# Optimization experiments

Measured on AMD Instinct MI355X. Metric: run time of the kernel, lower is better.

Reference implementation:

```python
import jax, jax.numpy as jnp
import numpy as np

B, MAXN, NVT, NINP, NHID, NHEAD, NL, NZ = 1024, 32, 16, 256, 512, 8, 6, 64
HID = MAXN * NHID
EPS = 1e-5
SCALE = 1.0 / np.sqrt(NHID // NHEAD)


def setup_inputs() -> dict:
    key = jax.random.key(0)
    ks = jax.random.split(key, 16)
    s = 0.02
    d = {}
    d["node_types"] = jax.random.randint(ks[0], (B, MAXN), 0, NVT, dtype=jnp.int32)
    d["adj_bits"] = jax.random.randint(ks[1], (B, MAXN, MAXN), 0, 2, dtype=jnp.int32)
    d["Wpos"] = jax.random.normal(ks[2], (MAXN, NINP), jnp.float32) * s
    d["bpos"] = jnp.zeros((NINP,), jnp.float32)
    d["Wnode"] = jax.random.normal(ks[3], (NVT, NINP), jnp.float32) * s
    d["bnode"] = jnp.zeros((NINP,), jnp.float32)
    for i, n in enumerate(["Wq", "Wk", "Wv", "Wo", "W1", "W2"]):
        d["enc_" + n] = jax.random.normal(ks[4 + i], (NL, NHID, NHID), jnp.float32) * s
    for n in ["bq", "bk", "bv", "bo", "b1", "b2"]:
        d["enc_" + n] = jnp.zeros((NL, NHID), jnp.float32)
    d["ln1_g"] = jnp.ones((NL, NHID), jnp.float32)
    d["ln1_b"] = jnp.zeros((NL, NHID), jnp.float32)
    d["ln2_g"] = jnp.ones((NL, NHID), jnp.float32)
    d["ln2_b"] = jnp.zeros((NL, NHID), jnp.float32)
    d["Wfc1"] = jax.random.normal(ks[10], (HID, NZ), jnp.float32) * s
    d["bfc1"] = jnp.zeros((NZ,), jnp.float32)
    d["Wfc2"] = jax.random.normal(ks[11], (HID, NZ), jnp.float32) * s
    d["bfc2"] = jnp.zeros((NZ,), jnp.float32)
    return d


def _ln(x, g, b):
    m = x.mean(-1, keepdims=True)
    v = ((x - m) ** 2).mean(-1, keepdims=True)
    return (x - m) * jax.lax.rsqrt(v + EPS) * g + b


def _dag_attn_bias(adj_bits):
    # _mask_generate: transitive closure via matmul powers; log-depth squaring
    # over a boolean semiring (min(.,1) after each add) gives identical reachability.
    iu = jnp.triu(jnp.ones((MAXN, MAXN), jnp.float32), 1)  # enforce DAG
    adj = adj_bits.astype(jnp.float32) * iu  # [B,N,N]
    reach = adj
    for _ in range(int(np.ceil(np.log2(MAXN)))):
        reach = jnp.minimum(reach + jnp.matmul(reach, reach), 1.0)
    # original: mask = (sum_powers + I) < 0.5 (True=disallowed), then transpose(1,2)
    allowed = (jnp.swapaxes(reach, 1, 2) + jnp.eye(MAXN, dtype=jnp.float32)) > 0.5
    return jnp.where(allowed, 0.0, -jnp.inf)[:, None, :, :]  # [B,1,N,N]


def _encode(node_types, adj_bits, Wpos, bpos, Wnode, bnode,
            enc_Wq, enc_bq, enc_Wk, enc_bk, enc_Wv, enc_bv, enc_Wo, enc_bo,
            ln1_g, ln1_b, enc_W1, enc_b1, enc_W2, enc_b2, ln2_g, ln2_b,
            Wfc1, bfc1, Wfc2, bfc2):
    node_feat = jax.nn.relu(Wnode[node_types] + bnode)               # [B,N,ninp]
    pos_feat = jnp.broadcast_to(Wpos + bpos, (B, MAXN, NINP))        # position = node index
    x = jnp.concatenate([node_feat, pos_feat], -1)                   # [B,N,512]
    bias = _dag_attn_bias(adj_bits)
    dh = NHID // NHEAD
    for l in range(NL):
        q = (x @ enc_Wq[l] + enc_bq[l]).reshape(B, MAXN, NHEAD, dh)
        k = (x @ enc_Wk[l] + enc_bk[l]).reshape(B, MAXN, NHEAD, dh)
        v = (x @ enc_Wv[l] + enc_bv[l]).reshape(B, MAXN, NHEAD, dh)
        s = jnp.einsum('bqhd,bkhd->bhqk', q, k) * SCALE + bias
        a = jax.nn.softmax(s, axis=-1)
        o = jnp.einsum('bhqk,bkhd->bqhd', a, v).reshape(B, MAXN, NHID)
        x = _ln(x + o @ enc_Wo[l] + enc_bo[l], ln1_g[l], ln1_b[l])    # post-LN
        f = jax.nn.relu(x @ enc_W1[l] + enc_b1[l]) @ enc_W2[l] + enc_b2[l]
        x = _ln(x + f, ln2_g[l], ln2_b[l])
    mem = x.reshape(B, HID)
    return mem @ Wfc1 + bfc1, mem @ Wfc2 + bfc2


def reference(node_types, adj_bits, Wpos, bpos, Wnode, bnode,
              enc_Wq, enc_bq, enc_Wk, enc_bk, enc_Wv, enc_bv, enc_Wo, enc_bo,
              ln1_g, ln1_b, enc_W1, enc_b1, enc_W2, enc_b2, ln2_g, ln2_b,
              Wfc1, bfc1, Wfc2, bfc2):
    return _encode(node_types, adj_bits, Wpos, bpos, Wnode, bnode,
                   enc_Wq, enc_bq, enc_Wk, enc_bk, enc_Wv, enc_bv, enc_Wo, enc_bo,
                   ln1_g, ln1_b, enc_W1, enc_b1, enc_W2, enc_b2, ln2_g, ln2_b,
                   Wfc1, bfc1, Wfc2, bfc2)
```

## Files before the change

kernel.cpp:

```cpp
#include <hip/hip_runtime.h>


typedef unsigned short u16;
typedef unsigned int u32;
typedef __attribute__((ext_vector_type(8))) short bf16x8;
typedef __attribute__((ext_vector_type(4))) float f32x4;

#define NB 1024
#define MAXN 32
#define NHID 512
#define NHEAD 8
#define NLAY 6
#define MTOT (NB * MAXN)
#define ATT_SCALE 0.125f
#define LN_EPS 1e-5f

__device__ __forceinline__ float bf2f(u16 h) { return __uint_as_float(((u32)h) << 16); }
__device__ __forceinline__ u16 f2bf(float f) {
  u32 u = __float_as_uint(f);
  return (u16)((u + 0x7fffu + ((u >> 16) & 1u)) >> 16);
}

__device__ __forceinline__ void gload16(const void* g, void* l) {
  __builtin_amdgcn_global_load_lds((const __attribute__((address_space(1))) void*)g,
                                   (__attribute__((address_space(3))) void*)l, 16, 0, 0);
}

__device__ __forceinline__ void xcd_remap(int l, int NX, int& mt, int& nt) {
  int xcd = l & 7;
  int s = l >> 3;
  int mg = s / NX;
  nt = s - mg * NX;
  mt = mg * 8 + xcd;
}

__global__ __launch_bounds__(256) void mask_k(const int* __restrict__ adj, u32* __restrict__ mask) {
  __shared__ u32 r[8][32];
  int tid = threadIdx.x;
  int g = tid >> 5, i = tid & 31;
  int b = blockIdx.x * 8 + g;
  const int* ab = adj + ((long)b * 32 + i) * 32;
  u32 m = 0;
  for (int j = i + 1; j < 32; ++j)
    if (ab[j]) m |= (1u << j);
  r[g][i] = m;
  __syncthreads();
  for (int it = 0; it < 5; ++it) {
    u32 cur = r[g][i];
    u32 acc = cur;
    #pragma unroll
    for (int j = 0; j < 32; ++j)
      if ((cur >> j) & 1u) acc |= r[g][j];
    __syncthreads();
    r[g][i] = acc;
    __syncthreads();
  }
  u32 am = 1u << i;
  #pragma unroll
  for (int k = 0; k < 32; ++k) am |= ((r[g][k] >> i) & 1u) << k;
  mask[b * 32 + i] = am;
}

__global__ __launch_bounds__(256) void embed_k(const int* __restrict__ types,
    const float* __restrict__ Wpos, const float* __restrict__ bpos,
    const float* __restrict__ Wnode, const float* __restrict__ bnode,
    u16* __restrict__ xb) {
  int i = blockIdx.x * 256 + threadIdx.x;
  int row = i >> 7, c = (i & 127) * 4;
  int b = row >> 5, n = row & 31;
  float v[4];
  if (c < 256) {
    int tp = types[b * 32 + n];
    const float* w = &Wnode[tp * 256 + c];
    #pragma unroll
    for (int j = 0; j < 4; ++j) v[j] = fmaxf(w[j] + bnode[c + j], 0.f);
  } else {
    int cc = c - 256;
    const float* w = &Wpos[n * 256 + cc];
    #pragma unroll
    for (int j = 0; j < 4; ++j) v[j] = w[j] + bpos[cc + j];
  }
  ushort4 h; h.x = f2bf(v[0]); h.y = f2bf(v[1]); h.z = f2bf(v[2]); h.w = f2bf(v[3]);
  *(ushort4*)&xb[(long)row * NHID + c] = h;
}

__global__ __launch_bounds__(256) void tconv_k(const float* __restrict__ W,
    u16* __restrict__ Wt, int n_off, int n_total) {
  __shared__ float tile[32][33];
  int l = blockIdx.z;
  int k0 = blockIdx.x * 32, n0 = blockIdx.y * 32;
  int tx = threadIdx.x & 31, ty = threadIdx.x >> 5;
  const float* src = W + (size_t)l * NHID * NHID;
  #pragma unroll
  for (int i = 0; i < 4; ++i)
    tile[ty + 8 * i][tx] = src[(size_t)(k0 + ty + 8 * i) * NHID + n0 + tx];
  __syncthreads();
  u16* dst = Wt + (size_t)l * n_total * NHID;
  #pragma unroll
  for (int i = 0; i < 4; ++i)
    dst[(size_t)(n_off + n0 + ty + 8 * i) * NHID + k0 + tx] = f2bf(tile[tx][ty + 8 * i]);
}

template <int EPI>
__global__ __launch_bounds__(256, 2) void gemm_bt(
    const u16* __restrict__ A, const u16* __restrict__ Bt,
    const float* __restrict__ bias0, const u16* __restrict__ res,
    u16* __restrict__ Cout, int N, int K) {
  __shared__ u16 As[128 * 32];
  __shared__ u16 Bs[128 * 32];
  const int tid = threadIdx.x;
  const int wave = tid >> 6, lane = tid & 63;
  int mt, nt;
  xcd_remap(blockIdx.x + gridDim.x * blockIdx.y, gridDim.x, mt, nt);
  const long m0 = (long)mt * 128;
  const int n0 = nt * 128;
  const int wr = wave >> 1, wc = wave & 1;
  const int srow = lane >> 2;
  const int sg = (lane & 3) ^ ((srow >> 1) & 3);
  const int fr = lane & 15;
  const int kq = lane >> 4;
  f32x4 acc[4][4] = {};

  const int kqx = (kq ^ ((fr >> 1) & 3)) * 8;
  for (int k0 = 0; k0 < K; k0 += 32) {
    #pragma unroll
    for (int i = 0; i < 2; ++i) {
      int c = 2 * wave + i;
      gload16(A + (m0 + 16 * c + srow) * (long)K + k0 + sg * 8, &As[c * 512]);
      gload16(Bt + (long)(n0 + 16 * c + srow) * K + k0 + sg * 8, &Bs[c * 512]);
    }
    __syncthreads();
    bf16x8 af[4], bfv[4];
    #pragma unroll
    for (int mi = 0; mi < 4; ++mi)
      af[mi] = *(const bf16x8*)&As[(wr * 64 + mi * 16 + fr) * 32 + kqx];
    #pragma unroll
    for (int ni = 0; ni < 4; ++ni)
      bfv[ni] = *(const bf16x8*)&Bs[(wc * 64 + ni * 16 + fr) * 32 + kqx];
    #pragma unroll
    for (int mi = 0; mi < 4; ++mi)
      #pragma unroll
      for (int ni = 0; ni < 4; ++ni)
        acc[mi][ni] = __builtin_amdgcn_mfma_f32_16x16x32_bf16(af[mi], bfv[ni], acc[mi][ni], 0, 0, 0);
    __syncthreads();
  }

  #pragma unroll
  for (int ni = 0; ni < 4; ++ni) {
    int n = n0 + wc * 64 + ni * 16 + fr;
    float bias = bias0[n];
    #pragma unroll
    for (int mi = 0; mi < 4; ++mi) {
      long r = m0 + wr * 64 + mi * 16 + kq * 4;
      #pragma unroll
      for (int j = 0; j < 4; ++j) {
        float v = acc[mi][ni][j] + bias;
        if (EPI == 2) v = fmaxf(v, 0.f);
        if (EPI == 3) v += bf2f(res[(r + j) * (long)N + n]);
        Cout[(r + j) * (long)N + n] = f2bf(v);
      }
    }
  }
}

template <int SWZ>
__global__ __launch_bounds__(256, 2) void gemm_qkv(
    const u16* __restrict__ A, const u16* __restrict__ Bt,
    const float* __restrict__ bq, const float* __restrict__ bk,
    const float* __restrict__ bv, u16* __restrict__ qk, u16* __restrict__ v) {
  __shared__ u16 As[128 * 32];
  __shared__ u16 Bs[128 * 32];
  const int tid = threadIdx.x;
  const int wave = tid >> 6, lane = tid & 63;
  int mt, nt;
  xcd_remap(blockIdx.x + gridDim.x * blockIdx.y, gridDim.x, mt, nt);
  const long m0 = (long)mt * 128;
  const int n0 = nt * 128;
  const int wr = wave >> 1, wc = wave & 1;
  const int srow = lane >> 2;
  const int sg = SWZ ? ((lane & 3) ^ ((srow >> 1) & 3)) : (lane & 3);
  const int fr = lane & 15;
  const int kq = lane >> 4;
  f32x4 acc[4][4] = {};

  const int kqx = SWZ ? ((kq ^ ((fr >> 1) & 3)) * 8) : (kq * 8);
  for (int k0 = 0; k0 < 512; k0 += 32) {
    #pragma unroll
    for (int i = 0; i < 2; ++i) {
      int c = 2 * wave + i;
      gload16(A + (m0 + 16 * c + srow) * 512L + k0 + sg * 8, &As[c * 512]);
      gload16(Bt + (long)(n0 + 16 * c + srow) * 512 + k0 + sg * 8, &Bs[c * 512]);
    }
    __syncthreads();
    bf16x8 af[4], bfv[4];
    #pragma unroll
    for (int mi = 0; mi < 4; ++mi)
      af[mi] = *(const bf16x8*)&As[(wr * 64 + mi * 16 + fr) * 32 + kqx];
    #pragma unroll
    for (int ni = 0; ni < 4; ++ni)
      bfv[ni] = *(const bf16x8*)&Bs[(wc * 64 + ni * 16 + fr) * 32 + kqx];
    #pragma unroll
    for (int mi = 0; mi < 4; ++mi)
      #pragma unroll
      for (int ni = 0; ni < 4; ++ni)
        acc[mi][ni] = __builtin_amdgcn_mfma_f32_16x16x32_bf16(af[mi], bfv[ni], acc[mi][ni], 0, 0, 0);
    __syncthreads();
  }

  #pragma unroll
  for (int ni = 0; ni < 4; ++ni) {
    int n = n0 + wc * 64 + ni * 16 + fr;
    float bias = (n < 512) ? bq[n] : ((n < 1024) ? bk[n - 512] : bv[n - 1024]);
    #pragma unroll
    for (int mi = 0; mi < 4; ++mi) {
      long r = m0 + wr * 64 + mi * 16 + kq * 4;
      #pragma unroll
      for (int j = 0; j < 4; ++j) {
        u16 hv = f2bf(acc[mi][ni][j] + bias);
        long rr = r + j;
        if (n < 1024) qk[rr * 1024 + n] = hv;
        else          v[rr * 512 + (n - 1024)] = hv;
      }
    }
  }
}

__global__ __launch_bounds__(256) void attn_k(const u16* __restrict__ qk,
    const u16* __restrict__ vfull, const u32* __restrict__ mask, u16* __restrict__ o) {
  __shared__ u16 vs_[4][64][40];
  __shared__ u16 p_lds[4][32][40];
  int tid = threadIdx.x;
  int w = tid >> 6, lane = tid & 63;
  int idx = blockIdx.x * 4 + w;
  int b = idx >> 3, h = idx & 7;
  const u16* qbase = qk + (long)b * 32 * 1024 + h * 64;
  const u16* kbase = qbase + 512;
  int g = lane >> 4, r = lane & 15;

  int node = lane >> 1, dh = lane & 1;
  const u16* vsrc = vfull + ((long)b * 32 + node) * 512 + h * 64 + dh * 32;
  bf16x8 vr[4];
  #pragma unroll
  for (int i = 0; i < 4; ++i) vr[i] = *(const bf16x8*)(vsrc + i * 8);

  f32x4 s[2][2] = {};
  #pragma unroll
  for (int ks = 0; ks < 2; ++ks) {
    bf16x8 kf[2], qf[2];
    #pragma unroll
    for (int mi = 0; mi < 2; ++mi)
      kf[mi] = *(const bf16x8*)(kbase + (long)(mi * 16 + r) * 1024 + ks * 32 + g * 8);
    #pragma unroll
    for (int nj = 0; nj < 2; ++nj)
      qf[nj] = *(const bf16x8*)(qbase + (long)(nj * 16 + r) * 1024 + ks * 32 + g * 8);
    #pragma unroll
    for (int mi = 0; mi < 2; ++mi)
      #pragma unroll
      for (int nj = 0; nj < 2; ++nj)
        s[mi][nj] = __builtin_amdgcn_mfma_f32_16x16x32_bf16(kf[mi], qf[nj], s[mi][nj], 0, 0, 0);
  }

  #pragma unroll
  for (int i = 0; i < 4; ++i)
    #pragma unroll
    for (int t = 0; t < 8; ++t)
      vs_[w][dh * 32 + i * 8 + t][node] = (u16)vr[i][t];

  #pragma unroll
  for (int nj = 0; nj < 2; ++nj) {
    int q = nj * 16 + r;
    u32 mk = mask[b * 32 + q];
    float vv[8];
    float mx = -1e30f;
    #pragma unroll
    for (int mi = 0; mi < 2; ++mi)
      #pragma unroll
      for (int j = 0; j < 4; ++j) {
        int k = mi * 16 + g * 4 + j;
        float val = ((mk >> k) & 1u) ? s[mi][nj][j] * ATT_SCALE : -1e30f;
        vv[mi * 4 + j] = val;
        mx = fmaxf(mx, val);
      }
    mx = fmaxf(mx, __shfl_xor(mx, 16));
    mx = fmaxf(mx, __shfl_xor(mx, 32));
    float sum = 0.f;
    #pragma unroll
    for (int i = 0; i < 8; ++i) { vv[i] = __expf(vv[i] - mx); sum += vv[i]; }
    sum += __shfl_xor(sum, 16);
    sum += __shfl_xor(sum, 32);
    float inv = 1.f / sum;
    #pragma unroll
    for (int mi = 0; mi < 2; ++mi) {
      ushort4 pk;
      pk.x = f2bf(vv[mi * 4 + 0] * inv);
      pk.y = f2bf(vv[mi * 4 + 1] * inv);
      pk.z = f2bf(vv[mi * 4 + 2] * inv);
      pk.w = f2bf(vv[mi * 4 + 3] * inv);
      *(ushort4*)&p_lds[w][q][mi * 16 + g * 4] = pk;
    }
  }

  bf16x8 pa[2];
  #pragma unroll
  for (int mi = 0; mi < 2; ++mi)
    pa[mi] = *(const bf16x8*)&p_lds[w][mi * 16 + r][g * 8];
  f32x4 oacc[2][4] = {};
  #pragma unroll
  for (int nd = 0; nd < 4; ++nd) {
    bf16x8 vf = *(const bf16x8*)&vs_[w][nd * 16 + r][g * 8];
    #pragma unroll
    for (int mi = 0; mi < 2; ++mi)
      oacc[mi][nd] = __builtin_amdgcn_mfma_f32_16x16x32_bf16(pa[mi], vf, oacc[mi][nd], 0, 0, 0);
  }
  #pragma unroll
  for (int mi = 0; mi < 2; ++mi)
    #pragma unroll
    for (int j = 0; j < 4; ++j) {
      int q = mi * 16 + g * 4 + j;
      u16* og = o + ((long)b * 32 + q) * NHID + h * 64;
      #pragma unroll
      for (int nd = 0; nd < 4; ++nd)
        og[nd * 16 + r] = f2bf(oacc[mi][nd][j]);
    }
}

__global__ __launch_bounds__(256) void ln_k(const u16* __restrict__ y,
    const float* __restrict__ g, const float* __restrict__ b, u16* __restrict__ xb) {
  int tid = threadIdx.x;
  int w = tid >> 6, lane = tid & 63;
  long row = (long)blockIdx.x * 4 + w;
  int c = lane * 8;
  long o = row * NHID + c;
  ushort4 a0 = *(const ushort4*)&y[o];
  ushort4 a1 = *(const ushort4*)&y[o + 4];
  float v[8] = {bf2f(a0.x), bf2f(a0.y), bf2f(a0.z), bf2f(a0.w),
                bf2f(a1.x), bf2f(a1.y), bf2f(a1.z), bf2f(a1.w)};
  float s = 0.f, sq = 0.f;
  #pragma unroll
  for (int j = 0; j < 8; ++j) { s += v[j]; sq += v[j] * v[j]; }
  #pragma unroll
  for (int off = 1; off < 64; off <<= 1) {
    s += __shfl_xor(s, off);
    sq += __shfl_xor(sq, off);
  }
  float mean = s * (1.f / 512.f);
  float inv = rsqrtf(sq * (1.f / 512.f) - mean * mean + LN_EPS);
  float4 ga = *(const float4*)&g[c], gb = *(const float4*)&g[c + 4];
  float4 ba = *(const float4*)&b[c], bb = *(const float4*)&b[c + 4];
  float gg[8] = {ga.x, ga.y, ga.z, ga.w, gb.x, gb.y, gb.z, gb.w};
  float bv[8] = {ba.x, ba.y, ba.z, ba.w, bb.x, bb.y, bb.z, bb.w};
  ushort4 o0, o1;
  o0.x = f2bf((v[0] - mean) * inv * gg[0] + bv[0]);
  o0.y = f2bf((v[1] - mean) * inv * gg[1] + bv[1]);
  o0.z = f2bf((v[2] - mean) * inv * gg[2] + bv[2]);
  o0.w = f2bf((v[3] - mean) * inv * gg[3] + bv[3]);
  o1.x = f2bf((v[4] - mean) * inv * gg[4] + bv[4]);
  o1.y = f2bf((v[5] - mean) * inv * gg[5] + bv[5]);
  o1.z = f2bf((v[6] - mean) * inv * gg[6] + bv[6]);
  o1.w = f2bf((v[7] - mean) * inv * gg[7] + bv[7]);
  *(ushort4*)&xb[o] = o0;
  *(ushort4*)&xb[o + 4] = o1;
}

__global__ __launch_bounds__(256) void fcT_k(const float* __restrict__ W1,
    const float* __restrict__ W2, u16* __restrict__ Wt) {
  __shared__ float t[64][65];
  int sel = blockIdx.y;
  const float* W = sel ? W2 : W1;
  int k0 = blockIdx.x * 64;
  int tx = threadIdx.x & 63, ty = threadIdx.x >> 6;
  #pragma unroll
  for (int i = 0; i < 16; ++i)
    t[ty + 4 * i][tx] = W[(long)(k0 + ty + 4 * i) * 64 + tx];
  __syncthreads();
  #pragma unroll
  for (int i = 0; i < 16; ++i)
    Wt[(long)(sel * 64 + ty + 4 * i) * 16384 + k0 + tx] = f2bf(t[tx][ty + 4 * i]);
}

__global__ __launch_bounds__(256, 2) void gemm_fc(const u16* __restrict__ A,
    const u16* __restrict__ Bt, float* __restrict__ part) {
  __shared__ u16 As[128 * 32];
  __shared__ u16 Bs[128 * 32];
  const int tid = threadIdx.x;
  const int wave = tid >> 6, lane = tid & 63;
  const int ks = blockIdx.x;
  const long m0 = (long)blockIdx.y * 128;
  const int kbase = ks * 512;
  const int wr = wave >> 1, wc = wave & 1;
  const int srow = lane >> 2;
  const int sg = (lane & 3) ^ ((srow >> 1) & 3);
  const int fr = lane & 15;
  const int kq = lane >> 4;
  f32x4 acc[4][4] = {};
  const int kqx = (kq ^ ((fr >> 1) & 3)) * 8;
  for (int k0 = 0; k0 < 512; k0 += 32) {
    #pragma unroll
    for (int i = 0; i < 2; ++i) {
      int c = 2 * wave + i;
      gload16(A + (m0 + 16 * c + srow) * 16384L + kbase + k0 + sg * 8, &As[c * 512]);
      gload16(Bt + (long)(16 * c + srow) * 16384L + kbase + k0 + sg * 8, &Bs[c * 512]);
    }
    __syncthreads();
    bf16x8 af[4], bfv[4];
    #pragma unroll
    for (int mi = 0; mi < 4; ++mi)
      af[mi] = *(const bf16x8*)&As[(wr * 64 + mi * 16 + fr) * 32 + kqx];
    #pragma unroll
    for (int ni = 0; ni < 4; ++ni)
      bfv[ni] = *(const bf16x8*)&Bs[(wc * 64 + ni * 16 + fr) * 32 + kqx];
    #pragma unroll
    for (int mi = 0; mi < 4; ++mi)
      #pragma unroll
      for (int ni = 0; ni < 4; ++ni)
        acc[mi][ni] = __builtin_amdgcn_mfma_f32_16x16x32_bf16(af[mi], bfv[ni], acc[mi][ni], 0, 0, 0);
    __syncthreads();
  }
  #pragma unroll
  for (int ni = 0; ni < 4; ++ni) {
    int n = wc * 64 + ni * 16 + fr;
    #pragma unroll
    for (int mi = 0; mi < 4; ++mi) {
      long rr = m0 + wr * 64 + mi * 16 + kq * 4;
      #pragma unroll
      for (int j = 0; j < 4; ++j)
        part[((long)ks * 1024 + rr + j) * 128 + n] = acc[mi][ni][j];
    }
  }
}

__global__ __launch_bounds__(256) void fc_red_k(const float* __restrict__ part,
    const float* __restrict__ bfc1, const float* __restrict__ bfc2,
    float* __restrict__ out) {
  int idx = blockIdx.x * 256 + threadIdx.x;
  int sel = idx >> 16;
  int rem = idx & 65535;
  int b = rem >> 6, z = rem & 63;
  float v = sel ? bfc2[z] : bfc1[z];
  #pragma unroll
  for (int ks = 0; ks < 32; ++ks)
    v += part[((long)ks * 1024 + b) * 128 + sel * 64 + z];
  out[idx] = v;
}

extern "C" void kernel_launch(void* const* d_in, const int* in_sizes, int n_in,
                              void* d_out, int out_size, void* d_ws, size_t ws_size,
                              hipStream_t stream) {
  const int* node_types = (const int*)d_in[0];
  const int* adj_bits = (const int*)d_in[1];
  const float* Wpos = (const float*)d_in[2];
  const float* bpos = (const float*)d_in[3];
  const float* Wnode = (const float*)d_in[4];
  const float* bnode = (const float*)d_in[5];
  const float* eWq = (const float*)d_in[6];
  const float* eWk = (const float*)d_in[7];
  const float* eWv = (const float*)d_in[8];
  const float* eWo = (const float*)d_in[9];
  const float* eW1 = (const float*)d_in[10];
  const float* eW2 = (const float*)d_in[11];
  const float* ebq = (const float*)d_in[12];
  const float* ebk = (const float*)d_in[13];
  const float* ebv = (const float*)d_in[14];
  const float* ebo = (const float*)d_in[15];
  const float* eb1 = (const float*)d_in[16];
  const float* eb2 = (const float*)d_in[17];
  const float* ln1g = (const float*)d_in[18];
  const float* ln1b = (const float*)d_in[19];
  const float* ln2g = (const float*)d_in[20];
  const float* ln2b = (const float*)d_in[21];
  const float* Wfc1 = (const float*)d_in[22];
  const float* bfc1 = (const float*)d_in[23];
  const float* Wfc2 = (const float*)d_in[24];
  const float* bfc2 = (const float*)d_in[25];

  char* ws = (char*)d_ws;
  size_t off = 0;
  auto carve = [&](size_t bytes) {
    void* p = ws + off;
    off += (bytes + 255) & ~(size_t)255;
    return p;
  };
  u16* Wqkv_t = (u16*)carve((size_t)NLAY * 1536 * 512 * 2);
  u16* Wo_t = (u16*)carve((size_t)NLAY * 512 * 512 * 2);
  u16* W1_t = (u16*)carve((size_t)NLAY * 512 * 512 * 2);
  u16* W2_t = (u16*)carve((size_t)NLAY * 512 * 512 * 2);
  u16* xb = (u16*)carve((size_t)MTOT * NHID * 2);
  u16* qk = (u16*)carve((size_t)MTOT * 1024 * 2);
  u16* vbuf = (u16*)carve((size_t)MTOT * NHID * 2);
  u16* obuf = (u16*)carve((size_t)MTOT * NHID * 2);
  u32* maskb = (u32*)carve((size_t)NB * MAXN * 4);
  u16* ybuf = qk;
  u16* hbuf = obuf;
  u16* Wt_fc = qk;
  float* part_fc = (float*)obuf;

  mask_k<<<NB / 8, 256, 0, stream>>>(adj_bits, maskb);
  embed_k<<<(MTOT * 128) / 256, 256, 0, stream>>>(node_types, Wpos, bpos, Wnode, bnode, xb);
  dim3 tg(16, 16, NLAY);
  tconv_k<<<tg, 256, 0, stream>>>(eWq, Wqkv_t, 0, 1536);
  tconv_k<<<tg, 256, 0, stream>>>(eWk, Wqkv_t, 512, 1536);
  tconv_k<<<tg, 256, 0, stream>>>(eWv, Wqkv_t, 1024, 1536);
  tconv_k<<<tg, 256, 0, stream>>>(eWo, Wo_t, 0, 512);
  tconv_k<<<tg, 256, 0, stream>>>(eW1, W1_t, 0, 512);
  tconv_k<<<tg, 256, 0, stream>>>(eW2, W2_t, 0, 512);

  for (int l = 0; l < NLAY; ++l) {
    size_t lw = (size_t)l * 512 * 512;
    if (l & 1)
      gemm_qkv<0><<<dim3(12, MTOT / 128), 256, 0, stream>>>(
          xb, Wqkv_t + (size_t)l * 1536 * 512,
          ebq + l * 512, ebk + l * 512, ebv + l * 512, qk, vbuf);
    else
      gemm_qkv<1><<<dim3(12, MTOT / 128), 256, 0, stream>>>(
          xb, Wqkv_t + (size_t)l * 1536 * 512,
          ebq + l * 512, ebk + l * 512, ebv + l * 512, qk, vbuf);
    attn_k<<<NB * NHEAD / 4, 256, 0, stream>>>(qk, vbuf, maskb, obuf);
    gemm_bt<3><<<dim3(4, MTOT / 128), 256, 0, stream>>>(
        obuf, Wo_t + lw, ebo + l * 512, xb, ybuf, 512, 512);
    ln_k<<<MTOT / 4, 256, 0, stream>>>(ybuf, ln1g + l * 512, ln1b + l * 512, xb);
    gemm_bt<2><<<dim3(4, MTOT / 128), 256, 0, stream>>>(
        xb, W1_t + lw, eb1 + l * 512, nullptr, hbuf, 512, 512);
    gemm_bt<3><<<dim3(4, MTOT / 128), 256, 0, stream>>>(
        hbuf, W2_t + lw, eb2 + l * 512, xb, ybuf, 512, 512);
    ln_k<<<MTOT / 4, 256, 0, stream>>>(ybuf, ln2g + l * 512, ln2b + l * 512, xb);
  }

  fcT_k<<<dim3(256, 2), 256, 0, stream>>>(Wfc1, Wfc2, Wt_fc);
  gemm_fc<<<dim3(32, 8), 256, 0, stream>>>(xb, Wt_fc, part_fc);
  fc_red_k<<<512, 256, 0, stream>>>(part_fc, bfc1, bfc2, (float*)d_out);
}
```

Measured before the change: 1.497 ms.

## Triple-buffer LDS in GEMM kernels with one barrier per k-step

```diff
diff --git a/kernel.cpp b/kernel.cpp
--- a/kernel.cpp
+++ b/kernel.cpp
@@ -101,19 +101,20 @@
     dst[(size_t)(n_off + n0 + ty + 8 * i) * NHID + k0 + tx] = f2bf(tile[tx][ty + 8 * i]);
 }
 
+
 template <int EPI>
 __global__ __launch_bounds__(256, 2) void gemm_bt(
     const u16* __restrict__ A, const u16* __restrict__ Bt,
     const float* __restrict__ bias0, const u16* __restrict__ res,
     u16* __restrict__ Cout, int N, int K) {
-  __shared__ u16 As[128 * 32];
-  __shared__ u16 Bs[128 * 32];
+  __shared__ u16 As[3][128 * 32];
+  __shared__ u16 Bs[3][128 * 32];
   const int tid = threadIdx.x;
   const int wave = tid >> 6, lane = tid & 63;
-  int mt, nt;
-  xcd_remap(blockIdx.x + gridDim.x * blockIdx.y, gridDim.x, mt, nt);
+  int mt, nt_;
+  xcd_remap(blockIdx.x + gridDim.x * blockIdx.y, gridDim.x, mt, nt_);
   const long m0 = (long)mt * 128;
-  const int n0 = nt * 128;
+  const int n0 = nt_ * 128;
   const int wr = wave >> 1, wc = wave & 1;
   const int srow = lane >> 2;
   const int sg = (lane & 3) ^ ((srow >> 1) & 3);
@@ -121,28 +122,43 @@
   const int kq = lane >> 4;
   f32x4 acc[4][4] = {};
 
-  const int kqx = (kq ^ ((fr >> 1) & 3)) * 8;
-  for (int k0 = 0; k0 < K; k0 += 32) {
+  auto stage = [&](int buf, int k0) {
     #pragma unroll
     for (int i = 0; i < 2; ++i) {
       int c = 2 * wave + i;
-      gload16(A + (m0 + 16 * c + srow) * (long)K + k0 + sg * 8, &As[c * 512]);
-      gload16(Bt + (long)(n0 + 16 * c + srow) * K + k0 + sg * 8, &Bs[c * 512]);
-    }
-    __syncthreads();
+      gload16(A + (m0 + 16 * c + srow) * (long)K + k0 + sg * 8, &As[buf][c * 512]);
+      gload16(Bt + (long)(n0 + 16 * c + srow) * K + k0 + sg * 8, &Bs[buf][c * 512]);
+    }
+  };
+  stage(0, 0);
+  stage(1, 32);
+  const int nt = K >> 5;
+  const int kqx = (kq ^ ((fr >> 1) & 3)) * 8;
+  int cs = 0;
+  #pragma unroll 1
+  for (int t = 0; t < nt; ++t) {
+    if (t + 1 < nt) asm volatile("s_waitcnt vmcnt(4)" ::: "memory");
+    else            asm volatile("s_waitcnt vmcnt(0)" ::: "memory");
+    __builtin_amdgcn_s_barrier();
+    if (t + 2 < nt) {
+      int nb = cs + 2; if (nb >= 3) nb -= 3;
+      stage(nb, (t + 2) * 32);
+    }
+    const u16* Asl = As[cs];
+    const u16* Bsl = Bs[cs];
     bf16x8 af[4], bfv[4];
     #pragma unroll
     for (int mi = 0; mi < 4; ++mi)
-      af[mi] = *(const bf16x8*)&As[(wr * 64 + mi * 16 + fr) * 32 + kqx];
+      af[mi] = *(const bf16x8*)&Asl[(wr * 64 + mi * 16 + fr) * 32 + kqx];
     #pragma unroll
     for (int ni = 0; ni < 4; ++ni)
-      bfv[ni] = *(const bf16x8*)&Bs[(wc * 64 + ni * 16 + fr) * 32 + kqx];
+      bfv[ni] = *(const bf16x8*)&Bsl[(wc * 64 + ni * 16 + fr) * 32 + kqx];
     #pragma unroll
     for (int mi = 0; mi < 4; ++mi)
       #pragma unroll
       for (int ni = 0; ni < 4; ++ni)
         acc[mi][ni] = __builtin_amdgcn_mfma_f32_16x16x32_bf16(af[mi], bfv[ni], acc[mi][ni], 0, 0, 0);
-    __syncthreads();
+    if (++cs == 3) cs = 0;
   }
 
   #pragma unroll
@@ -163,48 +179,61 @@
   }
 }
 
-template <int SWZ>
 __global__ __launch_bounds__(256, 2) void gemm_qkv(
     const u16* __restrict__ A, const u16* __restrict__ Bt,
     const float* __restrict__ bq, const float* __restrict__ bk,
     const float* __restrict__ bv, u16* __restrict__ qk, u16* __restrict__ v) {
-  __shared__ u16 As[128 * 32];
-  __shared__ u16 Bs[128 * 32];
+  __shared__ u16 As[3][128 * 32];
+  __shared__ u16 Bs[3][128 * 32];
   const int tid = threadIdx.x;
   const int wave = tid >> 6, lane = tid & 63;
-  int mt, nt;
-  xcd_remap(blockIdx.x + gridDim.x * blockIdx.y, gridDim.x, mt, nt);
+  int mt, nt_;
+  xcd_remap(blockIdx.x + gridDim.x * blockIdx.y, gridDim.x, mt, nt_);
   const long m0 = (long)mt * 128;
-  const int n0 = nt * 128;
+  const int n0 = nt_ * 128;
   const int wr = wave >> 1, wc = wave & 1;
   const int srow = lane >> 2;
-  const int sg = SWZ ? ((lane & 3) ^ ((srow >> 1) & 3)) : (lane & 3);
+  const int sg = (lane & 3) ^ ((srow >> 1) & 3);
   const int fr = lane & 15;
   const int kq = lane >> 4;
   f32x4 acc[4][4] = {};
 
-  const int kqx = SWZ ? ((kq ^ ((fr >> 1) & 3)) * 8) : (kq * 8);
-  for (int k0 = 0; k0 < 512; k0 += 32) {
+  auto stage = [&](int buf, int k0) {
     #pragma unroll
     for (int i = 0; i < 2; ++i) {
       int c = 2 * wave + i;
-      gload16(A + (m0 + 16 * c + srow) * 512L + k0 + sg * 8, &As[c * 512]);
-      gload16(Bt + (long)(n0 + 16 * c + srow) * 512 + k0 + sg * 8, &Bs[c * 512]);
-    }
-    __syncthreads();
+      gload16(A + (m0 + 16 * c + srow) * 512L + k0 + sg * 8, &As[buf][c * 512]);
+      gload16(Bt + (long)(n0 + 16 * c + srow) * 512 + k0 + sg * 8, &Bs[buf][c * 512]);
+    }
+  };
+  stage(0, 0);
+  stage(1, 32);
+  const int kqx = (kq ^ ((fr >> 1) & 3)) * 8;
+  int cs = 0;
+  #pragma unroll 1
+  for (int t = 0; t < 16; ++t) {
+    if (t + 1 < 16) asm volatile("s_waitcnt vmcnt(4)" ::: "memory");
+    else            asm volatile("s_waitcnt vmcnt(0)" ::: "memory");
+    __builtin_amdgcn_s_barrier();
+    if (t + 2 < 16) {
+      int nb = cs + 2; if (nb >= 3) nb -= 3;
+      stage(nb, (t + 2) * 32);
+    }
+    const u16* Asl = As[cs];
+    const u16* Bsl = Bs[cs];
     bf16x8 af[4], bfv[4];
     #pragma unroll
     for (int mi = 0; mi < 4; ++mi)
-      af[mi] = *(const bf16x8*)&As[(wr * 64 + mi * 16 + fr) * 32 + kqx];
+      af[mi] = *(const bf16x8*)&Asl[(wr * 64 + mi * 16 + fr) * 32 + kqx];
     #pragma unroll
     for (int ni = 0; ni < 4; ++ni)
-      bfv[ni] = *(const bf16x8*)&Bs[(wc * 64 + ni * 16 + fr) * 32 + kqx];
+      bfv[ni] = *(const bf16x8*)&Bsl[(wc * 64 + ni * 16 + fr) * 32 + kqx];
     #pragma unroll
     for (int mi = 0; mi < 4; ++mi)
       #pragma unroll
       for (int ni = 0; ni < 4; ++ni)
         acc[mi][ni] = __builtin_amdgcn_mfma_f32_16x16x32_bf16(af[mi], bfv[ni], acc[mi][ni], 0, 0, 0);
-    __syncthreads();
+    if (++cs == 3) cs = 0;
   }
 
   #pragma unroll
@@ -380,8 +409,8 @@
 
 __global__ __launch_bounds__(256, 2) void gemm_fc(const u16* __restrict__ A,
     const u16* __restrict__ Bt, float* __restrict__ part) {
-  __shared__ u16 As[128 * 32];
-  __shared__ u16 Bs[128 * 32];
+  __shared__ u16 As[3][128 * 32];
+  __shared__ u16 Bs[3][128 * 32];
   const int tid = threadIdx.x;
   const int wave = tid >> 6, lane = tid & 63;
   const int ks = blockIdx.x;
@@ -393,28 +422,42 @@
   const int fr = lane & 15;
   const int kq = lane >> 4;
   f32x4 acc[4][4] = {};
-  const int kqx = (kq ^ ((fr >> 1) & 3)) * 8;
-  for (int k0 = 0; k0 < 512; k0 += 32) {
+  auto stage = [&](int buf, int k0) {
     #pragma unroll
     for (int i = 0; i < 2; ++i) {
       int c = 2 * wave + i;
-      gload16(A + (m0 + 16 * c + srow) * 16384L + kbase + k0 + sg * 8, &As[c * 512]);
-      gload16(Bt + (long)(16 * c + srow) * 16384L + kbase + k0 + sg * 8, &Bs[c * 512]);
-    }
-    __syncthreads();
+      gload16(A + (m0 + 16 * c + srow) * 16384L + kbase + k0 + sg * 8, &As[buf][c * 512]);
+      gload16(Bt + (long)(16 * c + srow) * 16384L + kbase + k0 + sg * 8, &Bs[buf][c * 512]);
+    }
+  };
+  stage(0, 0);
+  stage(1, 32);
+  const int kqx = (kq ^ ((fr >> 1) & 3)) * 8;
+  int cs = 0;
+  #pragma unroll 1
+  for (int t = 0; t < 16; ++t) {
+    if (t + 1 < 16) asm volatile("s_waitcnt vmcnt(4)" ::: "memory");
+    else            asm volatile("s_waitcnt vmcnt(0)" ::: "memory");
+    __builtin_amdgcn_s_barrier();
+    if (t + 2 < 16) {
+      int nb = cs + 2; if (nb >= 3) nb -= 3;
+      stage(nb, (t + 2) * 32);
+    }
+    const u16* Asl = As[cs];
+    const u16* Bsl = Bs[cs];
     bf16x8 af[4], bfv[4];
     #pragma unroll
     for (int mi = 0; mi < 4; ++mi)
-      af[mi] = *(const bf16x8*)&As[(wr * 64 + mi * 16 + fr) * 32 + kqx];
+      af[mi] = *(const bf16x8*)&Asl[(wr * 64 + mi * 16 + fr) * 32 + kqx];
     #pragma unroll
     for (int ni = 0; ni < 4; ++ni)
-      bfv[ni] = *(const bf16x8*)&Bs[(wc * 64 + ni * 16 + fr) * 32 + kqx];
+      bfv[ni] = *(const bf16x8*)&Bsl[(wc * 64 + ni * 16 + fr) * 32 + kqx];
     #pragma unroll
     for (int mi = 0; mi < 4; ++mi)
       #pragma unroll
       for (int ni = 0; ni < 4; ++ni)
         acc[mi][ni] = __builtin_amdgcn_mfma_f32_16x16x32_bf16(af[mi], bfv[ni], acc[mi][ni], 0, 0, 0);
-    __syncthreads();
+    if (++cs == 3) cs = 0;
   }
   #pragma unroll
   for (int ni = 0; ni < 4; ++ni) {
@@ -506,14 +549,9 @@
 
   for (int l = 0; l < NLAY; ++l) {
     size_t lw = (size_t)l * 512 * 512;
-    if (l & 1)
-      gemm_qkv<0><<<dim3(12, MTOT / 128), 256, 0, stream>>>(
-          xb, Wqkv_t + (size_t)l * 1536 * 512,
-          ebq + l * 512, ebk + l * 512, ebv + l * 512, qk, vbuf);
-    else
-      gemm_qkv<1><<<dim3(12, MTOT / 128), 256, 0, stream>>>(
-          xb, Wqkv_t + (size_t)l * 1536 * 512,
-          ebq + l * 512, ebk + l * 512, ebv + l * 512, qk, vbuf);
+    gemm_qkv<<<dim3(12, MTOT / 128), 256, 0, stream>>>(
+        xb, Wqkv_t + (size_t)l * 1536 * 512,
+        ebq + l * 512, ebk + l * 512, ebv + l * 512, qk, vbuf);
     attn_k<<<NB * NHEAD / 4, 256, 0, stream>>>(qk, vbuf, maskb, obuf);
     gemm_bt<3><<<dim3(4, MTOT / 128), 256, 0, stream>>>(
         obuf, Wo_t + lw, ebo + l * 512, xb, ybuf, 512, 512);
```

Result: faster. 1.402 ms (-6.4%).
